# Kernel tuning notes

Measured on AMD Instinct MI355X. Metric: run time of the kernel, lower is better.

## Reference

```python
import jax, jax.numpy as jnp
import numpy as np

R = 16
ALPHA = 32
SCALING = ALPHA / R
SLOTS = 32
IN_F = 4096
OUT_F = 4096
B, T = 8, 1024


def setup_inputs() -> dict:
    key = jax.random.key(0)
    k1, k2, k3, k4, k5, k6 = jax.random.split(key, 6)
    x = jax.random.normal(k1, (B, T, IN_F), dtype=jnp.float32)
    adapter_mapping = jax.random.randint(k2, (B,), 0, SLOTS, dtype=jnp.int32)
    W = jax.random.normal(k3, (OUT_F, IN_F), dtype=jnp.float32) * 0.02
    b = jax.random.normal(k4, (OUT_F,), dtype=jnp.float32) * 0.02
    lora_As = jax.random.normal(k5, (SLOTS, IN_F, R), dtype=jnp.float32) * 0.02
    lora_Bs = jax.random.normal(k6, (SLOTS, R, OUT_F), dtype=jnp.float32) * 0.02
    return {"x": x, "adapter_mapping": adapter_mapping, "W": W, "b": b,
            "lora_As": lora_As, "lora_Bs": lora_Bs}


def reference(x, adapter_mapping, W, b, lora_As, lora_Bs):
    # base linear: y = x @ W.T + b
    base_out = jnp.einsum('bti,oi->bto', x, W) + b
    # per-example adapter gather (index_select along slot dim)
    A = lora_As[adapter_mapping]          # [B, in, r]
    Bm = lora_Bs[adapter_mapping]         # [B, r, out]
    lora_h = jnp.einsum('bti,bir->btr', x, A)
    lora_out = jnp.einsum('btr,bro->bto', lora_h, Bm)
    return base_out + lora_out * SCALING
```

## Files before the change

### kernel.cpp

```cpp
#include <hip/hip_runtime.h>
#include <hip/hip_bf16.h>


typedef __bf16 bf16_t;
typedef __bf16 bf16x8 __attribute__((ext_vector_type(8)));
typedef __bf16 bf16x4 __attribute__((ext_vector_type(4)));
typedef float f32x4 __attribute__((ext_vector_type(4)));

#define M_DIM 8192
#define K_DIM 4096
#define N_DIM 4096
#define SCALE_F 2.0f

__device__ __forceinline__ void gload_lds16(const void* g, void* l) {
    __builtin_amdgcn_global_load_lds(
        (const __attribute__((address_space(1))) void*)g,
        (__attribute__((address_space(3))) void*)l, 16, 0, 0);
}

__global__ __launch_bounds__(256) void cvt_kernel(const float* __restrict__ src,
                                                  bf16_t* __restrict__ dst, int n4) {
    int i = blockIdx.x * 256 + threadIdx.x;
    const int stride = gridDim.x * 256;
    for (; i < n4; i += stride) {
        f32x4 v = ((const f32x4*)src)[i];
        bf16x4 o = {(bf16_t)v[0], (bf16_t)v[1], (bf16_t)v[2], (bf16_t)v[3]};
        ((bf16x4*)dst)[i] = o;
    }
}

__global__ __launch_bounds__(256) void lora_hx_kernel(
    const float* __restrict__ X,
    const float* __restrict__ lora_As,
    const int* __restrict__ mapping,
    float* __restrict__ h_ws,
    bf16_t* __restrict__ Xb)
{
    __shared__ bf16_t Xt[32 * 16 * 8];
    __shared__ bf16_t At[16 * 136];
    __shared__ float hred[4 * 2 * 16 * 16];

    const int tid  = threadIdx.x;
    const int wave = tid >> 6;
    const int lane = tid & 63;
    const int bm0  = blockIdx.x * 32;
    const int slot = mapping[bm0 >> 10];
    const float* __restrict__ A = lora_As + (size_t)slot * (K_DIM * 16);

    const int srow = tid >> 3;
    const int sc2  = tid & 7;
    const int r16  = lane & 15;
    const int kq   = lane >> 4;

    f32x4 acc[2];
    acc[0] = (f32x4){0.f, 0.f, 0.f, 0.f};
    acc[1] = (f32x4){0.f, 0.f, 0.f, 0.f};

    for (int k0 = 0; k0 < K_DIM; k0 += 128) {
        const float* xp = X + (size_t)(bm0 + srow) * K_DIM + k0 + sc2 * 16;
        f32x4 v0 = *(const f32x4*)(xp);
        f32x4 v1 = *(const f32x4*)(xp + 4);
        f32x4 v2 = *(const f32x4*)(xp + 8);
        f32x4 v3 = *(const f32x4*)(xp + 12);
        bf16x8 c0 = {(bf16_t)v0[0], (bf16_t)v0[1], (bf16_t)v0[2], (bf16_t)v0[3],
                     (bf16_t)v1[0], (bf16_t)v1[1], (bf16_t)v1[2], (bf16_t)v1[3]};
        bf16x8 c1 = {(bf16_t)v2[0], (bf16_t)v2[1], (bf16_t)v2[2], (bf16_t)v2[3],
                     (bf16_t)v3[0], (bf16_t)v3[1], (bf16_t)v3[2], (bf16_t)v3[3]};
        if (Xb) {
            bf16x8* xbp = (bf16x8*)(Xb + (size_t)(bm0 + srow) * K_DIM + k0 + sc2 * 16);
            xbp[0] = c0;
            xbp[1] = c1;
        }
        const int k8a = sc2 * 2, k8b = sc2 * 2 + 1;
        *(bf16x8*)(Xt + (srow * 16 + (k8a ^ (srow & 15))) * 8) = c0;
        *(bf16x8*)(Xt + (srow * 16 + (k8b ^ (srow & 15))) * 8) = c1;

        {
            const int kk = tid >> 1, half = tid & 1;
            const float* ap = A + (size_t)(k0 + kk) * 16 + half * 8;
            f32x4 a0 = *(const f32x4*)ap;
            f32x4 a1 = *(const f32x4*)(ap + 4);
#pragma unroll
            for (int rr = 0; rr < 4; ++rr) {
                At[(half * 8 + rr) * 136 + kk]     = (bf16_t)a0[rr];
                At[(half * 8 + 4 + rr) * 136 + kk] = (bf16_t)a1[rr];
            }
        }
        __syncthreads();

#pragma unroll
        for (int i = 0; i < 2; ++i) {
            const int row_l = i * 16 + r16;
            const int c = wave * 4 + kq;
            bf16x8 af  = *(const bf16x8*)(Xt + (row_l * 16 + (c ^ (row_l & 15))) * 8);
            bf16x8 bfr = *(const bf16x8*)(At + r16 * 136 + wave * 32 + kq * 8);
            acc[i] = __builtin_amdgcn_mfma_f32_16x16x32_bf16(af, bfr, acc[i], 0, 0, 0);
        }
        __syncthreads();
    }

#pragma unroll
    for (int i = 0; i < 2; ++i)
#pragma unroll
        for (int e = 0; e < 4; ++e)
            hred[wave * 512 + i * 256 + (kq * 4 + e) * 16 + r16] = acc[i][e];
    __syncthreads();
#pragma unroll
    for (int q = 0; q < 2; ++q) {
        const int entry = tid * 2 + q;
        const int row_l = entry >> 4, col = entry & 15;
        const int i = row_l >> 4, rr = row_l & 15;
        const int off = i * 256 + rr * 16 + col;
        float s = hred[off] + hred[512 + off] + hred[1024 + off] + hred[1536 + off];
        h_ws[(size_t)(bm0 + row_l) * 16 + col] = s * SCALE_F;
    }
}

__device__ __forceinline__ void epilogue(
    f32x4 (&acc)[4][4], const float* __restrict__ bias,
    const float* __restrict__ lora_Bs, const int* __restrict__ mapping,
    const float* __restrict__ h_ws, float* __restrict__ out,
    int bm0, int bn0, int wm0, int wn0, int r16, int kq)
{
    const int slot = mapping[bm0 >> 10];
    const bool hasK = (kq < 2);
    const int kq2 = hasK ? kq : 0;

    bf16x8 hfrag[4], bmf[4];
#pragma unroll
    for (int i = 0; i < 4; ++i) {
        const float* hp = h_ws + (size_t)(bm0 + wm0 + i * 16 + r16) * 16 + kq2 * 8;
        f32x4 h0 = *(const f32x4*)hp;
        f32x4 h1 = *(const f32x4*)(hp + 4);
#pragma unroll
        for (int jj = 0; jj < 4; ++jj) {
            hfrag[i][jj]     = hasK ? (bf16_t)h0[jj] : (bf16_t)0.f;
            hfrag[i][jj + 4] = hasK ? (bf16_t)h1[jj] : (bf16_t)0.f;
        }
    }
#pragma unroll
    for (int j = 0; j < 4; ++j) {
        const int o = bn0 + wn0 + j * 16 + r16;
#pragma unroll
        for (int jj = 0; jj < 8; ++jj) {
            const int r = kq2 * 8 + jj;
            const float v = lora_Bs[((size_t)slot * 16 + r) * N_DIM + o];
            bmf[j][jj] = hasK ? (bf16_t)v : (bf16_t)0.f;
        }
    }
#pragma unroll
    for (int i = 0; i < 4; ++i)
#pragma unroll
        for (int j = 0; j < 4; ++j)
            acc[i][j] = __builtin_amdgcn_mfma_f32_16x16x32_bf16(hfrag[i], bmf[j], acc[i][j], 0, 0, 0);

#pragma unroll
    for (int j = 0; j < 4; ++j) {
        const int o = bn0 + wn0 + j * 16 + r16;
        const float bv = bias[o];
#pragma unroll
        for (int i = 0; i < 4; ++i) {
#pragma unroll
            for (int e = 0; e < 4; ++e) {
                const int m = bm0 + wm0 + i * 16 + kq * 4 + e;
                out[(size_t)m * N_DIM + o] = acc[i][j][e] + bv;
            }
        }
    }
}

__global__ __launch_bounds__(256) void gemm_lora_direct(
    const bf16_t* __restrict__ Xb, const bf16_t* __restrict__ Wb,
    const float* __restrict__ bias, const float* __restrict__ lora_Bs,
    const int* __restrict__ mapping, const float* __restrict__ h_ws,
    float* __restrict__ out)
{
    __shared__ bf16_t As[128 * 64];
    __shared__ bf16_t Bs[128 * 64];

    const int tid  = threadIdx.x;
    const int wave = tid >> 6;
    const int lane = tid & 63;
    const int bid  = blockIdx.x;
    const int n_t  = (bid & 7) + ((bid >> 9) << 3);
    const int m_t  = (bid >> 3) & 63;
    const int bm0 = m_t * 128;
    const int bn0 = n_t * 128;
    const int wm0 = (wave >> 1) * 64;
    const int wn0 = (wave & 1) * 64;
    const int r16 = lane & 15;
    const int kq  = lane >> 4;

    f32x4 acc[4][4];
#pragma unroll
    for (int i = 0; i < 4; ++i)
#pragma unroll
        for (int j = 0; j < 4; ++j) acc[i][j] = (f32x4){0.f, 0.f, 0.f, 0.f};

    for (int k0 = 0; k0 < K_DIM; k0 += 64) {
#pragma unroll
        for (int p = 0; p < 4; ++p) {
            const int base = wave * 256 + p * 64;
            const int s    = base + lane;
            const int row  = s >> 3;
            const int k8g  = (s & 7) ^ (row & 7);
            gload_lds16(Xb + (size_t)(bm0 + row) * K_DIM + k0 + k8g * 8,
                        As + (size_t)base * 8);
            gload_lds16(Wb + (size_t)(bn0 + row) * K_DIM + k0 + k8g * 8,
                        Bs + (size_t)base * 8);
        }
        __syncthreads();

#pragma unroll
        for (int kh = 0; kh < 2; ++kh) {
            bf16x8 af[4], bfr[4];
            const int k8 = kh * 4 + kq;
#pragma unroll
            for (int i = 0; i < 4; ++i) {
                const int ra = wm0 + i * 16 + r16;
                const int rb = wn0 + i * 16 + r16;
                af[i]  = *(const bf16x8*)(As + ((size_t)ra * 8 + (k8 ^ (ra & 7))) * 8);
                bfr[i] = *(const bf16x8*)(Bs + ((size_t)rb * 8 + (k8 ^ (rb & 7))) * 8);
            }
#pragma unroll
            for (int i = 0; i < 4; ++i)
#pragma unroll
                for (int j = 0; j < 4; ++j)
                    acc[i][j] = __builtin_amdgcn_mfma_f32_16x16x32_bf16(af[i], bfr[j], acc[i][j], 0, 0, 0);
        }
        __syncthreads();
    }

    epilogue(acc, bias, lora_Bs, mapping, h_ws, out, bm0, bn0, wm0, wn0, r16, kq);
}

__global__ __launch_bounds__(256) void gemm_lora_f32s(
    const float* __restrict__ Xf, const float* __restrict__ Wf,
    const float* __restrict__ bias, const float* __restrict__ lora_Bs,
    const int* __restrict__ mapping, const float* __restrict__ h_ws,
    float* __restrict__ out)
{
    __shared__ float Asf[128 * 32];
    __shared__ float Bsf[128 * 32];

    const int tid  = threadIdx.x;
    const int wave = tid >> 6;
    const int lane = tid & 63;
    const int bid  = blockIdx.x;
    const int n_t  = (bid & 7) + ((bid >> 9) << 3);
    const int m_t  = (bid >> 3) & 63;
    const int bm0 = m_t * 128;
    const int bn0 = n_t * 128;
    const int wm0 = (wave >> 1) * 64;
    const int wn0 = (wave & 1) * 64;
    const int r16 = lane & 15;
    const int kq  = lane >> 4;

    f32x4 acc[4][4];
#pragma unroll
    for (int i = 0; i < 4; ++i)
#pragma unroll
        for (int j = 0; j < 4; ++j) acc[i][j] = (f32x4){0.f, 0.f, 0.f, 0.f};

    for (int k0 = 0; k0 < K_DIM; k0 += 32) {
#pragma unroll
        for (int p = 0; p < 4; ++p) {
            const int idx0 = (p * 4 + wave) * 64;
            const int idx  = idx0 + lane;
            const int k4   = idx >> 7;
            const int row  = idx & 127;
            gload_lds16(Xf + (size_t)(bm0 + row) * K_DIM + (k0 + k4 * 4),
                        Asf + (size_t)idx0 * 4);
            gload_lds16(Wf + (size_t)(bn0 + row) * K_DIM + (k0 + k4 * 4),
                        Bsf + (size_t)idx0 * 4);
        }
        __syncthreads();

        bf16x8 af[4], bfr[4];
#pragma unroll
        for (int i = 0; i < 4; ++i) {
            const int ra = wm0 + i * 16 + r16;
            const int rb = wn0 + i * 16 + r16;
            f32x4 a0 = *(const f32x4*)(Asf + ((size_t)(kq * 2) * 128 + ra) * 4);
            f32x4 a1 = *(const f32x4*)(Asf + ((size_t)(kq * 2 + 1) * 128 + ra) * 4);
            f32x4 b0 = *(const f32x4*)(Bsf + ((size_t)(kq * 2) * 128 + rb) * 4);
            f32x4 b1 = *(const f32x4*)(Bsf + ((size_t)(kq * 2 + 1) * 128 + rb) * 4);
            af[i]  = (bf16x8){(bf16_t)a0[0], (bf16_t)a0[1], (bf16_t)a0[2], (bf16_t)a0[3],
                              (bf16_t)a1[0], (bf16_t)a1[1], (bf16_t)a1[2], (bf16_t)a1[3]};
            bfr[i] = (bf16x8){(bf16_t)b0[0], (bf16_t)b0[1], (bf16_t)b0[2], (bf16_t)b0[3],
                              (bf16_t)b1[0], (bf16_t)b1[1], (bf16_t)b1[2], (bf16_t)b1[3]};
        }
#pragma unroll
        for (int i = 0; i < 4; ++i)
#pragma unroll
            for (int j = 0; j < 4; ++j)
                acc[i][j] = __builtin_amdgcn_mfma_f32_16x16x32_bf16(af[i], bfr[j], acc[i][j], 0, 0, 0);
        __syncthreads();
    }

    epilogue(acc, bias, lora_Bs, mapping, h_ws, out, bm0, bn0, wm0, wn0, r16, kq);
}

extern "C" void kernel_launch(void* const* d_in, const int* in_sizes, int n_in,
                              void* d_out, int out_size, void* d_ws, size_t ws_size,
                              hipStream_t stream) {
    const float* x        = (const float*)d_in[0];
    const int*   mapping  = (const int*)d_in[1];
    const float* W        = (const float*)d_in[2];
    const float* b        = (const float*)d_in[3];
    const float* lora_As  = (const float*)d_in[4];
    const float* lora_Bs  = (const float*)d_in[5];
    float* out = (float*)d_out;

    const size_t xb_bytes = (size_t)M_DIM * K_DIM * 2;
    const size_t wb_bytes = (size_t)N_DIM * K_DIM * 2;
    const size_t h_bytes  = (size_t)M_DIM * 16 * 4;
    const bool direct = ws_size >= xb_bytes + wb_bytes + h_bytes;

    bf16_t* Xb = (bf16_t*)d_ws;
    bf16_t* Wb = (bf16_t*)((char*)d_ws + xb_bytes);
    float*  h_ws = direct ? (float*)((char*)d_ws + xb_bytes + wb_bytes)
                          : (float*)d_ws;

    lora_hx_kernel<<<dim3(M_DIM / 32), 256, 0, stream>>>(
        x, lora_As, mapping, h_ws, direct ? Xb : nullptr);

    if (direct) {
        cvt_kernel<<<dim3(2048), 256, 0, stream>>>(W, Wb, N_DIM * K_DIM / 4);
        gemm_lora_direct<<<dim3(2048), 256, 0, stream>>>(
            Xb, Wb, b, lora_Bs, mapping, h_ws, out);
    } else {
        gemm_lora_f32s<<<dim3(2048), 256, 0, stream>>>(
            x, W, b, lora_Bs, mapping, h_ws, out);
    }
}
```

Before: 652.2 us.

## Replace 128x128 GEMM with double-buffered 256x256 tile, 8-wave kernel

Replaces the bf16 direct GEMM with a 256x256-tile kernel using 512 threads (8 waves, each computing 128x64). LDS is double-buffered so the next K-tile's global-to-LDS loads are issued between MFMA phases, with s_setprio raised around MFMA bursts. The larger tile raises arithmetic intensity and halves global traffic per FLOP. In exchange it uses 128 KB of LDS per block and twice the accumulator registers, which limits occupancy, and leaves only 512 blocks for the grid.

```diff
diff --git a/kernel.cpp b/kernel.cpp
--- a/kernel.cpp
+++ b/kernel.cpp
@@ -11,6 +11,7 @@
 #define K_DIM 4096
 #define N_DIM 4096
 #define SCALE_F 2.0f
+#define NT (K_DIM / 64)
 
 __device__ __forceinline__ void gload_lds16(const void* g, void* l) {
     __builtin_amdgcn_global_load_lds(
@@ -169,14 +170,197 @@
     }
 }
 
-__global__ __launch_bounds__(256) void gemm_lora_direct(
+__device__ __forceinline__ void stage256(const bf16_t* __restrict__ G, int grow0, int k0,
+                                         bf16_t* lds, int wave, int lane) {
+#pragma unroll
+    for (int p = 0; p < 4; ++p) {
+        const int base = p * 512 + wave * 64;
+        const int s    = base + lane;
+        const int row  = s >> 3;
+        const int c    = (s & 7) ^ (row & 7);
+        gload_lds16(G + (size_t)(grow0 + row) * K_DIM + k0 + c * 8,
+                    lds + (size_t)base * 8);
+    }
+}
+
+__global__ __launch_bounds__(512, 2) void gemm_lora_256(
     const bf16_t* __restrict__ Xb, const bf16_t* __restrict__ Wb,
     const float* __restrict__ bias, const float* __restrict__ lora_Bs,
     const int* __restrict__ mapping, const float* __restrict__ h_ws,
     float* __restrict__ out)
 {
-    __shared__ bf16_t As[128 * 64];
-    __shared__ bf16_t Bs[128 * 64];
+    __shared__ bf16_t As[2][256 * 64];
+    __shared__ bf16_t Bs[2][256 * 64];
+
+    const int tid  = threadIdx.x;
+    const int wave = tid >> 6;
+    const int lane = tid & 63;
+    const int bid  = blockIdx.x;
+    const int wgid = (bid & 7) * 64 + (bid >> 3);
+    const int m_t  = wgid >> 4;
+    const int n_t  = wgid & 15;
+    const int bm0  = m_t * 256;
+    const int bn0  = n_t * 256;
+    const int wr   = wave >> 2;
+    const int wc   = wave & 3;
+    const int r16  = lane & 15;
+    const int kq   = lane >> 4;
+
+    f32x4 acc[8][4];
+#pragma unroll
+    for (int i = 0; i < 8; ++i)
+#pragma unroll
+        for (int j = 0; j < 4; ++j) acc[i][j] = (f32x4){0.f, 0.f, 0.f, 0.f};
+
+    stage256(Xb, bm0, 0, As[0], wave, lane);
+    stage256(Wb, bn0, 0, Bs[0], wave, lane);
+    asm volatile("s_waitcnt vmcnt(0)" ::: "memory");
+    __builtin_amdgcn_s_barrier();
+
+#pragma unroll 2
+    for (int t = 0; t < NT; ++t) {
+        const int b = t & 1;
+        const bf16_t* Ab = As[b];
+        const bf16_t* Bb = Bs[b];
+        bf16_t* An = As[b ^ 1];
+        bf16_t* Bn = Bs[b ^ 1];
+        const bool pre = (t + 1 < NT);
+        const int k0n  = (t + 1) * 64;
+
+        bf16x8 af[4], bfr[4];
+
+#pragma unroll
+        for (int i = 0; i < 4; ++i) {
+            const int ra = wr * 128 + i * 16 + r16;
+            af[i] = *(const bf16x8*)(Ab + ((size_t)ra * 8 + (kq ^ (ra & 7))) * 8);
+        }
+#pragma unroll
+        for (int j = 0; j < 4; ++j) {
+            const int rb = wc * 64 + j * 16 + r16;
+            bfr[j] = *(const bf16x8*)(Bb + ((size_t)rb * 8 + (kq ^ (rb & 7))) * 8);
+        }
+        if (pre) stage256(Xb, bm0, k0n, An, wave, lane);
+        __builtin_amdgcn_s_barrier();
+        __builtin_amdgcn_s_setprio(1);
+#pragma unroll
+        for (int i = 0; i < 4; ++i)
+#pragma unroll
+            for (int j = 0; j < 4; ++j)
+                acc[i][j] = __builtin_amdgcn_mfma_f32_16x16x32_bf16(af[i], bfr[j], acc[i][j], 0, 0, 0);
+        __builtin_amdgcn_s_setprio(0);
+        __builtin_amdgcn_s_barrier();
+
+#pragma unroll
+        for (int i = 0; i < 4; ++i) {
+            const int ra = wr * 128 + 64 + i * 16 + r16;
+            af[i] = *(const bf16x8*)(Ab + ((size_t)ra * 8 + (kq ^ (ra & 7))) * 8);
+        }
+        if (pre) stage256(Wb, bn0, k0n, Bn, wave, lane);
+        __builtin_amdgcn_s_barrier();
+        __builtin_amdgcn_s_setprio(1);
+#pragma unroll
+        for (int i = 0; i < 4; ++i)
+#pragma unroll
+            for (int j = 0; j < 4; ++j)
+                acc[4 + i][j] = __builtin_amdgcn_mfma_f32_16x16x32_bf16(af[i], bfr[j], acc[4 + i][j], 0, 0, 0);
+        __builtin_amdgcn_s_setprio(0);
+        __builtin_amdgcn_s_barrier();
+
+#pragma unroll
+        for (int i = 0; i < 4; ++i) {
+            const int ra = wr * 128 + i * 16 + r16;
+            af[i] = *(const bf16x8*)(Ab + ((size_t)ra * 8 + ((4 + kq) ^ (ra & 7))) * 8);
+        }
+#pragma unroll
+        for (int j = 0; j < 4; ++j) {
+            const int rb = wc * 64 + j * 16 + r16;
+            bfr[j] = *(const bf16x8*)(Bb + ((size_t)rb * 8 + ((4 + kq) ^ (rb & 7))) * 8);
+        }
+        __builtin_amdgcn_s_barrier();
+        __builtin_amdgcn_s_setprio(1);
+#pragma unroll
+        for (int i = 0; i < 4; ++i)
+#pragma unroll
+            for (int j = 0; j < 4; ++j)
+                acc[i][j] = __builtin_amdgcn_mfma_f32_16x16x32_bf16(af[i], bfr[j], acc[i][j], 0, 0, 0);
+        __builtin_amdgcn_s_setprio(0);
+        __builtin_amdgcn_s_barrier();
+
+#pragma unroll
+        for (int i = 0; i < 4; ++i) {
+            const int ra = wr * 128 + 64 + i * 16 + r16;
+            af[i] = *(const bf16x8*)(Ab + ((size_t)ra * 8 + ((4 + kq) ^ (ra & 7))) * 8);
+        }
+        __builtin_amdgcn_s_barrier();
+        __builtin_amdgcn_s_setprio(1);
+#pragma unroll
+        for (int i = 0; i < 4; ++i)
+#pragma unroll
+            for (int j = 0; j < 4; ++j)
+                acc[4 + i][j] = __builtin_amdgcn_mfma_f32_16x16x32_bf16(af[i], bfr[j], acc[4 + i][j], 0, 0, 0);
+        __builtin_amdgcn_s_setprio(0);
+        if (pre) {
+            asm volatile("s_waitcnt vmcnt(0)" ::: "memory");
+        }
+        __builtin_amdgcn_s_barrier();
+    }
+
+    const int slot = mapping[bm0 >> 10];
+    const bool hasK = (kq < 2);
+    const int kq2 = hasK ? kq : 0;
+    const int wm0 = wr * 128, wn0 = wc * 64;
+
+    bf16x8 hfrag[8], bmf[4];
+#pragma unroll
+    for (int i = 0; i < 8; ++i) {
+        const float* hp = h_ws + (size_t)(bm0 + wm0 + i * 16 + r16) * 16 + kq2 * 8;
+        f32x4 h0 = *(const f32x4*)hp;
+        f32x4 h1 = *(const f32x4*)(hp + 4);
+#pragma unroll
+        for (int jj = 0; jj < 4; ++jj) {
+            hfrag[i][jj]     = hasK ? (bf16_t)h0[jj] : (bf16_t)0.f;
+            hfrag[i][jj + 4] = hasK ? (bf16_t)h1[jj] : (bf16_t)0.f;
+        }
+    }
+#pragma unroll
+    for (int j = 0; j < 4; ++j) {
+        const int o = bn0 + wn0 + j * 16 + r16;
+#pragma unroll
+        for (int jj = 0; jj < 8; ++jj) {
+            const int r = kq2 * 8 + jj;
+            const float v = lora_Bs[((size_t)slot * 16 + r) * N_DIM + o];
+            bmf[j][jj] = hasK ? (bf16_t)v : (bf16_t)0.f;
+        }
+    }
+#pragma unroll
+    for (int i = 0; i < 8; ++i)
+#pragma unroll
+        for (int j = 0; j < 4; ++j)
+            acc[i][j] = __builtin_amdgcn_mfma_f32_16x16x32_bf16(hfrag[i], bmf[j], acc[i][j], 0, 0, 0);
+
+#pragma unroll
+    for (int j = 0; j < 4; ++j) {
+        const int o = bn0 + wn0 + j * 16 + r16;
+        const float bv = bias[o];
+#pragma unroll
+        for (int i = 0; i < 8; ++i) {
+#pragma unroll
+            for (int e = 0; e < 4; ++e) {
+                const int m = bm0 + wm0 + i * 16 + kq * 4 + e;
+                out[(size_t)m * N_DIM + o] = acc[i][j][e] + bv;
+            }
+        }
+    }
+}
+
+__global__ __launch_bounds__(256) void gemm_lora_f32s(
+    const float* __restrict__ Xf, const float* __restrict__ Wf,
+    const float* __restrict__ bias, const float* __restrict__ lora_Bs,
+    const int* __restrict__ mapping, const float* __restrict__ h_ws,
+    float* __restrict__ out)
+{
+    __shared__ float Asf[128 * 32];
+    __shared__ float Bsf[128 * 32];
 
     const int tid  = threadIdx.x;
     const int wave = tid >> 6;
@@ -197,71 +381,6 @@
 #pragma unroll
         for (int j = 0; j < 4; ++j) acc[i][j] = (f32x4){0.f, 0.f, 0.f, 0.f};
 
-    for (int k0 = 0; k0 < K_DIM; k0 += 64) {
-#pragma unroll
-        for (int p = 0; p < 4; ++p) {
-            const int base = wave * 256 + p * 64;
-            const int s    = base + lane;
-            const int row  = s >> 3;
-            const int k8g  = (s & 7) ^ (row & 7);
-            gload_lds16(Xb + (size_t)(bm0 + row) * K_DIM + k0 + k8g * 8,
-                        As + (size_t)base * 8);
-            gload_lds16(Wb + (size_t)(bn0 + row) * K_DIM + k0 + k8g * 8,
-                        Bs + (size_t)base * 8);
-        }
-        __syncthreads();
-
-#pragma unroll
-        for (int kh = 0; kh < 2; ++kh) {
-            bf16x8 af[4], bfr[4];
-            const int k8 = kh * 4 + kq;
-#pragma unroll
-            for (int i = 0; i < 4; ++i) {
-                const int ra = wm0 + i * 16 + r16;
-                const int rb = wn0 + i * 16 + r16;
-                af[i]  = *(const bf16x8*)(As + ((size_t)ra * 8 + (k8 ^ (ra & 7))) * 8);
-                bfr[i] = *(const bf16x8*)(Bs + ((size_t)rb * 8 + (k8 ^ (rb & 7))) * 8);
-            }
-#pragma unroll
-            for (int i = 0; i < 4; ++i)
-#pragma unroll
-                for (int j = 0; j < 4; ++j)
-                    acc[i][j] = __builtin_amdgcn_mfma_f32_16x16x32_bf16(af[i], bfr[j], acc[i][j], 0, 0, 0);
-        }
-        __syncthreads();
-    }
-
-    epilogue(acc, bias, lora_Bs, mapping, h_ws, out, bm0, bn0, wm0, wn0, r16, kq);
-}
-
-__global__ __launch_bounds__(256) void gemm_lora_f32s(
-    const float* __restrict__ Xf, const float* __restrict__ Wf,
-    const float* __restrict__ bias, const float* __restrict__ lora_Bs,
-    const int* __restrict__ mapping, const float* __restrict__ h_ws,
-    float* __restrict__ out)
-{
-    __shared__ float Asf[128 * 32];
-    __shared__ float Bsf[128 * 32];
-
-    const int tid  = threadIdx.x;
-    const int wave = tid >> 6;
-    const int lane = tid & 63;
-    const int bid  = blockIdx.x;
-    const int n_t  = (bid & 7) + ((bid >> 9) << 3);
-    const int m_t  = (bid >> 3) & 63;
-    const int bm0 = m_t * 128;
-    const int bn0 = n_t * 128;
-    const int wm0 = (wave >> 1) * 64;
-    const int wn0 = (wave & 1) * 64;
-    const int r16 = lane & 15;
-    const int kq  = lane >> 4;
-
-    f32x4 acc[4][4];
-#pragma unroll
-    for (int i = 0; i < 4; ++i)
-#pragma unroll
-        for (int j = 0; j < 4; ++j) acc[i][j] = (f32x4){0.f, 0.f, 0.f, 0.f};
-
     for (int k0 = 0; k0 < K_DIM; k0 += 32) {
 #pragma unroll
         for (int p = 0; p < 4; ++p) {
@@ -327,7 +446,7 @@
 
     if (direct) {
         cvt_kernel<<<dim3(2048), 256, 0, stream>>>(W, Wb, N_DIM * K_DIM / 4);
-        gemm_lora_direct<<<dim3(2048), 256, 0, stream>>>(
+        gemm_lora_256<<<dim3((M_DIM / 256) * (N_DIM / 256)), 512, 0, stream>>>(
             Xb, Wb, b, lora_Bs, mapping, h_ws, out);
     } else {
         gemm_lora_f32s<<<dim3(2048), 256, 0, stream>>>(
```

Measured after the change: 681.4 us. +4.5%, slower.

## Merge W conversion into LoRA prep kernel and prefetch next X/A tile

Applied to the files above, without the earlier changes.

Combines the W fp32-to-bf16 conversion and the LoRA x·A projection into one launch, with block ranges split between the two jobs so they run concurrently and a kernel launch is removed. Inside the LoRA path, the next k-tile of X and A is loaded into registers right after the barrier, overlapping global loads with the MFMA step (software prefetch). This costs extra registers, and the W-conversion blocks compete with the LoRA blocks for bandwidth.

```diff
diff --git a/kernel.cpp b/kernel.cpp
--- a/kernel.cpp
+++ b/kernel.cpp
@@ -12,38 +12,49 @@
 #define N_DIM 4096
 #define SCALE_F 2.0f
 
+#define LORA_BLOCKS 256
+#define CVT_BLOCKS 2048
+#define PREP_BLOCKS (LORA_BLOCKS + CVT_BLOCKS)
+
 __device__ __forceinline__ void gload_lds16(const void* g, void* l) {
     __builtin_amdgcn_global_load_lds(
         (const __attribute__((address_space(1))) void*)g,
         (__attribute__((address_space(3))) void*)l, 16, 0, 0);
 }
 
-__global__ __launch_bounds__(256) void cvt_kernel(const float* __restrict__ src,
-                                                  bf16_t* __restrict__ dst, int n4) {
-    int i = blockIdx.x * 256 + threadIdx.x;
-    const int stride = gridDim.x * 256;
-    for (; i < n4; i += stride) {
-        f32x4 v = ((const f32x4*)src)[i];
-        bf16x4 o = {(bf16_t)v[0], (bf16_t)v[1], (bf16_t)v[2], (bf16_t)v[3]};
-        ((bf16x4*)dst)[i] = o;
-    }
-}
-
-__global__ __launch_bounds__(256) void lora_hx_kernel(
+__global__ __launch_bounds__(256) void prep_kernel(
     const float* __restrict__ X,
     const float* __restrict__ lora_As,
     const int* __restrict__ mapping,
     float* __restrict__ h_ws,
-    bf16_t* __restrict__ Xb)
+    bf16_t* __restrict__ Xb,
+    const float* __restrict__ W,
+    bf16_t* __restrict__ Wb)
 {
     __shared__ bf16_t Xt[32 * 16 * 8];
     __shared__ bf16_t At[16 * 136];
     __shared__ float hred[4 * 2 * 16 * 16];
 
-    const int tid  = threadIdx.x;
+    const int tid = threadIdx.x;
+    const int bid = blockIdx.x;
+
+    if (bid >= LORA_BLOCKS) {
+        if (Wb) {
+            const int n4 = N_DIM * K_DIM / 4;
+            int i = (bid - LORA_BLOCKS) * 256 + tid;
+            const int stride = CVT_BLOCKS * 256;
+            for (; i < n4; i += stride) {
+                f32x4 v = ((const f32x4*)W)[i];
+                bf16x4 o = {(bf16_t)v[0], (bf16_t)v[1], (bf16_t)v[2], (bf16_t)v[3]};
+                ((bf16x4*)Wb)[i] = o;
+            }
+        }
+        return;
+    }
+
     const int wave = tid >> 6;
     const int lane = tid & 63;
-    const int bm0  = blockIdx.x * 32;
+    const int bm0  = bid * 32;
     const int slot = mapping[bm0 >> 10];
     const float* __restrict__ A = lora_As + (size_t)slot * (K_DIM * 16);
 
@@ -51,21 +62,27 @@
     const int sc2  = tid & 7;
     const int r16  = lane & 15;
     const int kq   = lane >> 4;
+    const int kk   = tid >> 1;
+    const int half = tid & 1;
 
     f32x4 acc[2];
     acc[0] = (f32x4){0.f, 0.f, 0.f, 0.f};
     acc[1] = (f32x4){0.f, 0.f, 0.f, 0.f};
 
+    const float* xrow = X + (size_t)(bm0 + srow) * K_DIM + sc2 * 16;
+
+    f32x4 xv0 = *(const f32x4*)(xrow);
+    f32x4 xv1 = *(const f32x4*)(xrow + 4);
+    f32x4 xv2 = *(const f32x4*)(xrow + 8);
+    f32x4 xv3 = *(const f32x4*)(xrow + 12);
+    f32x4 av0 = *(const f32x4*)(A + (size_t)kk * 16 + half * 8);
+    f32x4 av1 = *(const f32x4*)(A + (size_t)kk * 16 + half * 8 + 4);
+
     for (int k0 = 0; k0 < K_DIM; k0 += 128) {
-        const float* xp = X + (size_t)(bm0 + srow) * K_DIM + k0 + sc2 * 16;
-        f32x4 v0 = *(const f32x4*)(xp);
-        f32x4 v1 = *(const f32x4*)(xp + 4);
-        f32x4 v2 = *(const f32x4*)(xp + 8);
-        f32x4 v3 = *(const f32x4*)(xp + 12);
-        bf16x8 c0 = {(bf16_t)v0[0], (bf16_t)v0[1], (bf16_t)v0[2], (bf16_t)v0[3],
-                     (bf16_t)v1[0], (bf16_t)v1[1], (bf16_t)v1[2], (bf16_t)v1[3]};
-        bf16x8 c1 = {(bf16_t)v2[0], (bf16_t)v2[1], (bf16_t)v2[2], (bf16_t)v2[3],
-                     (bf16_t)v3[0], (bf16_t)v3[1], (bf16_t)v3[2], (bf16_t)v3[3]};
+        bf16x8 c0 = {(bf16_t)xv0[0], (bf16_t)xv0[1], (bf16_t)xv0[2], (bf16_t)xv0[3],
+                     (bf16_t)xv1[0], (bf16_t)xv1[1], (bf16_t)xv1[2], (bf16_t)xv1[3]};
+        bf16x8 c1 = {(bf16_t)xv2[0], (bf16_t)xv2[1], (bf16_t)xv2[2], (bf16_t)xv2[3],
+                     (bf16_t)xv3[0], (bf16_t)xv3[1], (bf16_t)xv3[2], (bf16_t)xv3[3]};
         if (Xb) {
             bf16x8* xbp = (bf16x8*)(Xb + (size_t)(bm0 + srow) * K_DIM + k0 + sc2 * 16);
             xbp[0] = c0;
@@ -75,18 +92,23 @@
         *(bf16x8*)(Xt + (srow * 16 + (k8a ^ (srow & 15))) * 8) = c0;
         *(bf16x8*)(Xt + (srow * 16 + (k8b ^ (srow & 15))) * 8) = c1;
 
-        {
-            const int kk = tid >> 1, half = tid & 1;
-            const float* ap = A + (size_t)(k0 + kk) * 16 + half * 8;
-            f32x4 a0 = *(const f32x4*)ap;
-            f32x4 a1 = *(const f32x4*)(ap + 4);
-#pragma unroll
-            for (int rr = 0; rr < 4; ++rr) {
-                At[(half * 8 + rr) * 136 + kk]     = (bf16_t)a0[rr];
-                At[(half * 8 + 4 + rr) * 136 + kk] = (bf16_t)a1[rr];
-            }
-        }
-        __syncthreads();
+#pragma unroll
+        for (int rr = 0; rr < 4; ++rr) {
+            At[(half * 8 + rr) * 136 + kk]     = (bf16_t)av0[rr];
+            At[(half * 8 + 4 + rr) * 136 + kk] = (bf16_t)av1[rr];
+        }
+        __syncthreads();
+
+        if (k0 + 128 < K_DIM) {
+            const float* xp = xrow + k0 + 128;
+            xv0 = *(const f32x4*)(xp);
+            xv1 = *(const f32x4*)(xp + 4);
+            xv2 = *(const f32x4*)(xp + 8);
+            xv3 = *(const f32x4*)(xp + 12);
+            const float* ap = A + (size_t)(k0 + 128 + kk) * 16 + half * 8;
+            av0 = *(const f32x4*)ap;
+            av1 = *(const f32x4*)(ap + 4);
+        }
 
 #pragma unroll
         for (int i = 0; i < 2; ++i) {
@@ -322,11 +344,11 @@
     float*  h_ws = direct ? (float*)((char*)d_ws + xb_bytes + wb_bytes)
                           : (float*)d_ws;
 
-    lora_hx_kernel<<<dim3(M_DIM / 32), 256, 0, stream>>>(
-        x, lora_As, mapping, h_ws, direct ? Xb : nullptr);
+    prep_kernel<<<dim3(PREP_BLOCKS), 256, 0, stream>>>(
+        x, lora_As, mapping, h_ws,
+        direct ? Xb : nullptr, W, direct ? Wb : nullptr);
 
     if (direct) {
-        cvt_kernel<<<dim3(2048), 256, 0, stream>>>(W, Wb, N_DIM * K_DIM / 4);
         gemm_lora_direct<<<dim3(2048), 256, 0, stream>>>(
             Xb, Wb, b, lora_Bs, mapping, h_ws, out);
     } else {
```

Result: slower. 721.8 us (+10.7%).
